# Performance work log

Hardware: AMD Instinct MI355X
Metric: run time of the kernel (lower is better)

Reference implementation:

```python
import jax, jax.numpy as jnp
import numpy as np
import math

B, C_IN, S, D, H, L, FF = 16, 32, 512, 256, 8, 4, 1024
HD = D // H
EPS = 1e-5


def setup_inputs() -> dict:
    key = jax.random.key(0)
    ks = jax.random.split(key, 32)
    r = lambda k, shp: jax.random.normal(k, shp, dtype=jnp.float32) * 0.02
    inp = {
        'x': jax.random.normal(ks[0], (B, C_IN, S), dtype=jnp.float32),
        'conv1_w': r(ks[1], (D, C_IN, 7)), 'conv1_b': jnp.zeros((D,)),
        'bn1_g': jnp.ones((D,)), 'bn1_b': jnp.zeros((D,)),
        'conv2_w': r(ks[2], (D, D, 5)), 'conv2_b': jnp.zeros((D,)),
        'bn2_g': jnp.ones((D,)), 'bn2_b': jnp.zeros((D,)),
        'ln1_g': jnp.ones((L, D)), 'ln1_b': jnp.zeros((L, D)),
        'wq': r(ks[3], (L, D, D)), 'wk': r(ks[4], (L, D, D)),
        'wv': r(ks[5], (L, D, D)), 'wo': r(ks[6], (L, D, D)),
        'bo': jnp.zeros((L, D)),
        'bias_table': r(ks[7], (L, 2 * S - 1, H)),
        'ln2_g': jnp.ones((L, D)), 'ln2_b': jnp.zeros((L, D)),
        'w1': r(ks[8], (L, D, FF)), 'b1': jnp.zeros((L, FF)),
        'w2': r(ks[9], (L, FF, D)), 'b2': jnp.zeros((L, D)),
        'fn_g': jnp.ones((D,)), 'fn_b': jnp.zeros((D,)),
    }
    return inp


def _conv1d(x, w, b, pad):
    # x: (B, C, T), w: (O, I, K) -> (B, O, T)
    y = jax.lax.conv_general_dilated(x, w, (1,), [(pad, pad)],
                                     dimension_numbers=('NCH', 'OIH', 'NCH'))
    return y + b[None, :, None]


def _bn_eval(x, g, b):
    # eval-mode batchnorm with running mean 0, var 1
    return x * (g / jnp.sqrt(1.0 + EPS))[None, :, None] + b[None, :, None]


def _ln(x, g, b):
    mu = jnp.mean(x, axis=-1, keepdims=True)
    var = jnp.var(x, axis=-1, keepdims=True)
    return (x - mu) / jnp.sqrt(var + EPS) * g + b


def _pos_encoding():
    pos = np.arange(S, dtype=np.float32)[:, None]
    div = np.exp(np.arange(0, D, 2, dtype=np.float32) * (-math.log(10000.0) / D))
    scale = D / S
    pe = np.zeros((S, D), dtype=np.float32)
    pe[:, 0::2] = np.sin(pos * div * scale)
    pe[:, 1::2] = np.cos(pos * div * scale)
    return jnp.asarray(pe)


_REL_IDX = jnp.asarray(np.arange(S)[:, None] - np.arange(S)[None, :] + S - 1)  # (S,S)
_PE = _pos_encoding()


def reference(x, conv1_w, conv1_b, bn1_g, bn1_b, conv2_w, conv2_b, bn2_g, bn2_b,
              ln1_g, ln1_b, wq, wk, wv, wo, bo, bias_table,
              ln2_g, ln2_b, w1, b1, w2, b2, fn_g, fn_b):
    # tokenizer
    h = jax.nn.gelu(_bn_eval(_conv1d(x, conv1_w, conv1_b, 3), bn1_g, bn1_b), approximate=False)
    h = jax.nn.gelu(_bn_eval(_conv1d(h, conv2_w, conv2_b, 2), bn2_g, bn2_b), approximate=False)
    t = jnp.transpose(h, (0, 2, 1))  # (B, S, D)
    # positional encoding
    t = t + _PE[None, :, :]
    scale = HD ** -0.5
    for i in range(L):
        xn = _ln(t, ln1_g[i], ln1_b[i])
        q = (xn @ wq[i]).reshape(B, S, H, HD)
        k = (xn @ wk[i]).reshape(B, S, H, HD)
        v = (xn @ wv[i]).reshape(B, S, H, HD)
        scores = jnp.einsum('bihd,bjhd->bhij', q, k) * scale
        rel = bias_table[i][_REL_IDX]              # (S, S, H)
        scores = scores + jnp.transpose(rel, (2, 0, 1))[None]
        probs = jax.nn.softmax(scores, axis=-1)
        ctx = jnp.einsum('bhij,bjhd->bihd', probs, v).reshape(B, S, D)
        t = t + ctx @ wo[i] + bo[i]
        xn2 = _ln(t, ln2_g[i], ln2_b[i])
        ff = jax.nn.gelu(xn2 @ w1[i] + b1[i], approximate=False) @ w2[i] + b2[i]
        t = t + ff
    return _ln(t, fn_g, fn_b)
```

## Files before the change

kernel.cpp:

```cpp
#include <hip/hip_runtime.h>
#include <hip/hip_bf16.h>
#include <stdint.h>

#define B_   16
#define CIN_ 32
#define S_   512
#define D_   256
#define H_   8
#define L_   4
#define FF_  1024
#define HD_  32
#define EPS_ 1e-5f

typedef __hip_bfloat16 bf16;
typedef __attribute__((ext_vector_type(8))) short short8;
typedef __attribute__((ext_vector_type(4))) float floatx4;

__device__ __forceinline__ float b2f(bf16 v) { return __bfloat162float(v); }
__device__ __forceinline__ bf16 f2b(float v) { return __float2bfloat16(v); }
__device__ __forceinline__ float gelu_f(float v) {
    return 0.5f * v * (1.0f + erff(v * 0.70710678118654752f));
}
__device__ __forceinline__ float pe_val(int s, int d) {
    int m2 = d & ~1;
    float div = expf((float)m2 * (-9.210340371976184f / 256.0f));
    float ang = (float)s * div * 0.5f;
    return (d & 1) ? cosf(ang) : sinf(ang);
}
__device__ __forceinline__ float us2f(unsigned short u) {
    return __uint_as_float(((unsigned)u) << 16);
}

__device__ __forceinline__ void wtrans_tile(const float* __restrict__ src, bf16* __restrict__ dst,
                                            int K, int N, int n0, int k0, int rowoff,
                                            const float* __restrict__ gvec,
                                            float (*tile)[33], int tid) {
    int tx = tid & 31, ty0 = tid >> 5;
#pragma unroll
    for (int r = 0; r < 4; ++r) {
        int ky = r * 8 + ty0;
        tile[ky][tx] = src[(long)(k0 + ky) * N + n0 + tx];
    }
    __syncthreads();
    float gs = gvec ? gvec[k0 + tx] : 1.0f;
#pragma unroll
    for (int r = 0; r < 4; ++r) {
        int ny = r * 8 + ty0;
        dst[(long)(rowoff + n0 + ny) * K + k0 + tx] = f2b(tile[tx][ny] * gs);
    }
}

__global__ void prep_kernel(const float* __restrict__ wq, const float* __restrict__ wk,
                            const float* __restrict__ wv, const float* __restrict__ wo,
                            const float* __restrict__ w1, const float* __restrict__ w2,
                            const float* __restrict__ ln1_g, const float* __restrict__ ln1_b,
                            const float* __restrict__ ln2_g, const float* __restrict__ ln2_b,
                            bf16* __restrict__ wqkvT, bf16* __restrict__ woT,
                            bf16* __restrict__ w1T, bf16* __restrict__ w2T,
                            const float* __restrict__ w1c, const float* __restrict__ cb1,
                            const float* __restrict__ g1, const float* __restrict__ bb1,
                            const float* __restrict__ w2c, const float* __restrict__ cb2,
                            const float* __restrict__ g2, const float* __restrict__ bb2,
                            bf16* __restrict__ c1w, bf16* __restrict__ c2w,
                            float* __restrict__ sh1, float* __restrict__ sh2,
                            float* __restrict__ zpage,
                            float* __restrict__ gWq, float* __restrict__ bWq,
                            float* __restrict__ gWf, float* __restrict__ bWf) {
    __shared__ float tile[32][33];
    int tid = threadIdx.x;
    int bid = blockIdx.x;
    if (bid < 3072) {
        int l = bid / 768, r = bid % 768;
        if (r < 256) {
            int which = r >> 6, rr = r & 63;
            int n0 = (rr & 7) * 32, k0 = (rr >> 3) * 32;
            const float* s = (which == 0 ? wq : which == 1 ? wk : which == 2 ? wv : wo) + (long)l * 65536;
            bf16* d = (which == 3) ? (woT + (long)l * 65536) : (wqkvT + (long)l * 768 * 256);
            const float* gv = (which == 3) ? nullptr : (ln1_g + l * 256);
            wtrans_tile(s, d, 256, 256, n0, k0, (which == 3) ? 0 : which * 256, gv, tile, tid);
        } else if (r < 512) {
            int rr = r - 256;
            int n0 = (rr & 31) * 32, k0 = (rr >> 5) * 32;
            wtrans_tile(w1 + (long)l * 262144, w1T + (long)l * 262144, 256, 1024, n0, k0, 0,
                        ln2_g + l * 256, tile, tid);
        } else {
            int rr = r - 512;
            int n0 = (rr & 7) * 32, k0 = (rr >> 3) * 32;
            wtrans_tile(w2 + (long)l * 262144, w2T + (long)l * 262144, 1024, 256, n0, k0, 0,
                        nullptr, tile, tid);
        }
        return;
    }
    if (bid >= 3105) {
        int j = bid - 3105;
        int l = j / 7, r = j % 7;
        int n = tid;
        if (r < 3) {
            const float* W = (r == 0 ? wq : r == 1 ? wk : wv) + (long)l * 65536;
            const float* g = ln1_g + l * 256;
            const float* bb = ln1_b + l * 256;
            float sg = 0.0f, sb = 0.0f;
            for (int k = 0; k < 256; ++k) {
                float w = W[k * 256 + n];
                sg += g[k] * w;
                sb += bb[k] * w;
            }
            gWq[l * 768 + r * 256 + n] = sg;
            bWq[l * 768 + r * 256 + n] = sb;
        } else {
            int c = r - 3;
            const float* W = w1 + (long)l * 262144;
            const float* g = ln2_g + l * 256;
            const float* bb = ln2_b + l * 256;
            float sg = 0.0f, sb = 0.0f;
            for (int k = 0; k < 256; ++k) {
                float w = W[k * 1024 + c * 256 + n];
                sg += g[k] * w;
                sb += bb[k] * w;
            }
            gWf[l * 1024 + c * 256 + n] = sg;
            bWf[l * 1024 + c * 256 + n] = sb;
        }
        return;
    }
    int cb = bid - 3072;
    int ty = tid >> 4, t16 = tid & 15;
    float rinv = rsqrtf(1.0f + EPS_);
    if (cb < 16) {
        int o = cb * 16 + ty;
        float scale = g1[o] * rinv;
        if (t16 == 0) sh1[o] = cb1[o] * scale + bb1[o];
        for (int j = t16; j < 256; j += 16) {
            int kk = j >> 5, i = j & 31;
            float v = (kk < 7) ? w1c[o * 224 + i * 7 + kk] * scale : 0.0f;
            c1w[o * 256 + kk * 32 + i] = f2b(v);
        }
    } else if (cb < 32) {
        int o = (cb - 16) * 16 + ty;
        float scale = g2[o] * rinv;
        if (t16 == 0) sh2[o] = cb2[o] * scale + bb2[o];
        for (int j = t16; j < D_ * 5; j += 16) {
            int i = j / 5, kk = j % 5;
            c2w[o * 1280 + kk * 256 + i] = f2b(w2c[o * 1280 + i * 5 + kk] * scale);
        }
    } else {
        if (tid < 64) zpage[tid] = 0.0f;
    }
}

__global__ void im2col1_kernel(const float* __restrict__ x, bf16* __restrict__ col) {
    int kk = blockIdx.x, b = blockIdx.y;
    for (int t = threadIdx.x; t < 512 * 32; t += 256) {
        int s = t & 511, i = t >> 9;
        int sp = s + kk - 3;
        float v = (kk < 7 && sp >= 0 && sp < 512) ? x[((b << 5) + i) * 512 + sp] : 0.0f;
        col[(long)((b << 9) + s) * 256 + kk * 32 + i] = f2b(v);
    }
}

__global__ void ln_kernel(const float* __restrict__ x, const float* __restrict__ g,
                          const float* __restrict__ bt, float* __restrict__ out_f) {
    int row = blockIdx.x;
    int tid = threadIdx.x;
    float v = x[(long)row * D_ + tid];
    float s1 = v, s2 = v * v;
    __shared__ float red[8];
#pragma unroll
    for (int off = 32; off; off >>= 1) {
        s1 += __shfl_xor(s1, off);
        s2 += __shfl_xor(s2, off);
    }
    int wave = tid >> 6;
    if ((tid & 63) == 0) { red[wave] = s1; red[4 + wave] = s2; }
    __syncthreads();
    if (tid == 0) {
        float a = red[0] + red[1] + red[2] + red[3];
        float q = red[4] + red[5] + red[6] + red[7];
        float mu = a * (1.0f / D_);
        float var = q * (1.0f / D_) - mu * mu;
        red[0] = mu;
        red[1] = rsqrtf(var + EPS_);
    }
    __syncthreads();
    out_f[(long)row * D_ + tid] = (v - red[0]) * red[1] * g[tid] + bt[tid];
}

template <int ROWS>
__device__ __forceinline__ void stage_sw(const char* gbase, long rs_bytes, int k_byte_off,
                                         char* lds_base, int tid) {
    constexpr int ROUNDS = ROWS / 32;
    char* lp = lds_base + (tid & 192) * 16;
#pragma unroll
    for (int r = 0; r < ROUNDS; ++r) {
        int s = r * 256 + tid;
        int row = s >> 3;
        int q = ((s & 7) ^ (row & 7)) * 16;
        const char* gp = gbase + (long)row * rs_bytes + k_byte_off + q;
        __builtin_amdgcn_global_load_lds((const __attribute__((address_space(1))) void*)gp,
                                         (__attribute__((address_space(3))) void*)(lp + r * 4096),
                                         16, 0, 0);
    }
}
__device__ __forceinline__ int sw_off(int m, int qc) {
    return m * 128 + ((qc ^ (m & 7)) * 16);
}

__device__ __forceinline__ void stage_c2(const char* h1b, int s0, int kt, const char* zp,
                                         char* lds_base, int tid) {
    int kk = kt >> 2;
    int c0 = (kt & 3) * 128;
    char* lp = lds_base + (tid & 192) * 16;
    int row = tid >> 3;
    int q = ((tid & 7) ^ (row & 7)) * 16;
    int sp = s0 + row + kk - 2;
    const char* gp = (sp >= 0 && sp < 512) ? h1b + (long)sp * 512 + c0 + q : zp + q;
    __builtin_amdgcn_global_load_lds((const __attribute__((address_space(1))) void*)gp,
                                     (__attribute__((address_space(3))) void*)lp, 16, 0, 0);
}

enum { FB = 1, FG = 2, FR = 4, FO16 = 8, FLN = 16, FW16 = 32 };

template <int BM, int NB, int FLAGS, bool VT>
__global__ __launch_bounds__(256) void gemm_sw(const bf16* __restrict__ A, const bf16* __restrict__ Wt,
                                               const float* __restrict__ bias, const float* __restrict__ res,
                                               const float* __restrict__ gW, const float* __restrict__ bW,
                                               float* __restrict__ outf, bf16* __restrict__ outb,
                                               bf16* __restrict__ out16, bf16* __restrict__ vt,
                                               int M, int N, int K) {
    constexpr int FM = BM / 32;
    __shared__ __align__(16) short As[2][BM * 64];
    __shared__ __align__(16) short Bs[2][64 * 64];
    __shared__ float mus[64], rstds[64];
    int tid = threadIdx.x;
    int wave = tid >> 6, lane = tid & 63;
    int frow = lane & 15, fquad = lane >> 4;
    int id = blockIdx.x;
    int m_low = id & 7;
    int s = id >> 3;
    int ni = s % NB;
    int mi = (s / NB) * 8 + m_low;
    int m0 = mi * BM, n0 = ni * 64;
    int wm = (wave & 1) * (BM / 2), wn = (wave >> 1) * 32;
    floatx4 acc[FM][2] = {};
    const char* Ab = (const char*)A + (long)m0 * K * 2;
    const char* Bb = (const char*)Wt + (long)n0 * K * 2;
    long rs = (long)K * 2;
    int KT = K >> 6;
    float s1 = 0.0f, s2 = 0.0f;
    int srow = tid >> 2, spart = tid & 3;
    stage_sw<BM>(Ab, rs, 0, (char*)As[0], tid);
    stage_sw<64>(Bb, rs, 0, (char*)Bs[0], tid);
    for (int kt = 0; kt < KT; ++kt) {
        int cur = kt & 1;
        __syncthreads();
        if (kt + 1 < KT) {
            stage_sw<BM>(Ab, rs, (kt + 1) * 128, (char*)As[1 - cur], tid);
            stage_sw<64>(Bb, rs, (kt + 1) * 128, (char*)Bs[1 - cur], tid);
        }
        const char* Ap = (const char*)As[cur];
        const char* Bp = (const char*)Bs[cur];
        if (FLAGS & FLN) {
#pragma unroll
            for (int c = 0; c < 2; ++c) {
                short8 v8 = *(const short8*)(Ap + sw_off(srow, spart * 2 + c));
#pragma unroll
                for (int e = 0; e < 8; ++e) {
                    float f = us2f((unsigned short)v8[e]);
                    s1 += f;
                    s2 += f * f;
                }
            }
        }
#pragma unroll
        for (int kh = 0; kh < 2; ++kh) {
            short8 af[FM], bw[2];
#pragma unroll
            for (int i = 0; i < FM; ++i)
                af[i] = *(const short8*)(Ap + sw_off(wm + i * 16 + frow, kh * 4 + fquad));
#pragma unroll
            for (int j = 0; j < 2; ++j)
                bw[j] = *(const short8*)(Bp + sw_off(wn + j * 16 + frow, kh * 4 + fquad));
#pragma unroll
            for (int i = 0; i < FM; ++i)
#pragma unroll
                for (int j = 0; j < 2; ++j)
                    acc[i][j] = __builtin_amdgcn_mfma_f32_16x16x32_bf16(af[i], bw[j], acc[i][j], 0, 0, 0);
        }
    }
    if (FLAGS & FLN) {
        s1 += __shfl_xor(s1, 1); s1 += __shfl_xor(s1, 2);
        s2 += __shfl_xor(s2, 1); s2 += __shfl_xor(s2, 2);
        if (spart == 0) {
            float mu = s1 * (1.0f / 256.0f);
            float var = s2 * (1.0f / 256.0f) - mu * mu;
            mus[srow] = mu;
            rstds[srow] = rsqrtf(var + EPS_);
        }
        __syncthreads();
    }
#pragma unroll
    for (int i = 0; i < FM; ++i) {
#pragma unroll
        for (int j = 0; j < 2; ++j) {
#pragma unroll
            for (int r = 0; r < 4; ++r) {
                int rl = wm + i * 16 + fquad * 4 + r;
                int row = m0 + rl;
                int col = n0 + wn + j * 16 + frow;
                float v = acc[i][j][r];
                if (FLAGS & FLN) {
                    float rsd = rstds[rl], mm = mus[rl];
                    v = v * rsd - rsd * mm * gW[col] + bW[col];
                }
                if (FLAGS & FB) v += bias[col];
                if (FLAGS & FG) v = gelu_f(v);
                if (FLAGS & FR) v += res[(long)row * N + col];
                if (VT) {
                    if (col < 512) {
                        outb[(long)row * 512 + col] = f2b(v);
                    } else {
                        int h = (col - 512) >> 5, d = col & 31;
                        int b = row >> 9, ss = row & 511;
                        vt[(long)((b * 8 + h) * 32 + d) * 512 + ss] = f2b(v);
                    }
                } else if (FLAGS & FO16) {
                    outb[(long)row * N + col] = f2b(v);
                } else {
                    outf[(long)row * N + col] = v;
                }
                if (FLAGS & FW16) out16[(long)row * N + col] = f2b(v);
            }
        }
    }
}

template <int NB>
__global__ __launch_bounds__(256) void gemm_c2(const bf16* __restrict__ h1, const bf16* __restrict__ c2w,
                                               const float* __restrict__ sh2, const float* __restrict__ zp,
                                               float* __restrict__ outf, bf16* __restrict__ out16) {
    __shared__ __align__(16) short As[2][32 * 64];
    __shared__ __align__(16) short Bs[2][64 * 64];
    int tid = threadIdx.x;
    int wave = tid >> 6, lane = tid & 63;
    int frow = lane & 15, fquad = lane >> 4;
    int id = blockIdx.x;
    int m_low = id & 7;
    int sdec = id >> 3;
    int ni = sdec % NB;
    int mi = (sdec / NB) * 8 + m_low;
    int m0 = mi * 32, n0 = ni * 64;
    int bb = m0 >> 9, s0 = m0 & 511;
    int wm = (wave & 1) * 16, wn = (wave >> 1) * 32;
    floatx4 acc[2] = {};
    const char* h1b = (const char*)h1 + (long)bb * 512 * 512;
    const char* Bb = (const char*)c2w + (long)n0 * 2560;
    stage_c2(h1b, s0, 0, (const char*)zp, (char*)As[0], tid);
    stage_sw<64>(Bb, 2560, 0, (char*)Bs[0], tid);
    for (int kt = 0; kt < 20; ++kt) {
        int cur = kt & 1;
        __syncthreads();
        if (kt + 1 < 20) {
            stage_c2(h1b, s0, kt + 1, (const char*)zp, (char*)As[1 - cur], tid);
            stage_sw<64>(Bb, 2560, (kt + 1) * 128, (char*)Bs[1 - cur], tid);
        }
        const char* Ap = (const char*)As[cur];
        const char* Bp = (const char*)Bs[cur];
#pragma unroll
        for (int kh = 0; kh < 2; ++kh) {
            short8 af, bw[2];
            af = *(const short8*)(Ap + sw_off(wm + frow, kh * 4 + fquad));
#pragma unroll
            for (int j = 0; j < 2; ++j)
                bw[j] = *(const short8*)(Bp + sw_off(wn + j * 16 + frow, kh * 4 + fquad));
#pragma unroll
            for (int j = 0; j < 2; ++j)
                acc[j] = __builtin_amdgcn_mfma_f32_16x16x32_bf16(af, bw[j], acc[j], 0, 0, 0);
        }
    }
#pragma unroll
    for (int j = 0; j < 2; ++j) {
#pragma unroll
        for (int r = 0; r < 4; ++r) {
            int row = m0 + wm + fquad * 4 + r;
            int col = n0 + wn + j * 16 + frow;
            float v = gelu_f(acc[j][r] + sh2[col]) + pe_val(row & 511, col);
            outf[(long)row * 256 + col] = v;
            out16[(long)row * 256 + col] = f2b(v);
        }
    }
}

#define PSTR2 72
__device__ __forceinline__ void stage_k(const char* gK, int j0, char* dst, int tid) {
    char* lp = dst + (tid & 192) * 16;
#pragma unroll
    for (int r = 0; r < 2; ++r) {
        int l = r * 256 + tid;
        int sr = l >> 3, cp = l & 7;
        int c = cp ^ (sr & 7);
        int j = sr * 2 + (c >> 2), cj = c & 3;
        const char* gp = gK + (long)(j0 + j) * 1024 + cj * 16;
        __builtin_amdgcn_global_load_lds((const __attribute__((address_space(1))) void*)gp,
                                         (__attribute__((address_space(3))) void*)(lp + r * 4096), 16, 0, 0);
    }
}
__device__ __forceinline__ void stage_v(const char* gV, int j0, char* dst, int tid) {
    char* lp = dst + (tid & 192) * 16;
#pragma unroll
    for (int r = 0; r < 2; ++r) {
        int l = r * 256 + tid;
        int row = l >> 4, cp = l & 15;
        int c = cp ^ (row & 7);
        const char* gp = gV + (long)row * 1024 + j0 * 2 + c * 16;
        __builtin_amdgcn_global_load_lds((const __attribute__((address_space(1))) void*)gp,
                                         (__attribute__((address_space(3))) void*)(lp + r * 4096), 16, 0, 0);
    }
}

__global__ __launch_bounds__(256) void fattn_kernel(const bf16* __restrict__ qk,
                                                    const bf16* __restrict__ Vt,
                                                    const float* __restrict__ bias_l,
                                                    bf16* __restrict__ ctx) {
    __shared__ __align__(16) char Ks[2][8192];
    __shared__ __align__(16) char Vs[2][8192];
    __shared__ __align__(16) short Ps[4 * 32 * PSTR2];
    __shared__ float bias_s[640];
    int tid = threadIdx.x;
    int wave = tid >> 6, lane = tid & 63;
    int frow = lane & 15, fquad = lane >> 4;
    int bh = blockIdx.y;
    int b = bh >> 3, h = bh & 7;
    int i0 = blockIdx.x * 128;
    int wm = wave * 32;
    const float scale = 0.17677669529663687f;

    for (int t = tid; t < 639; t += 256) bias_s[t] = bias_l[(i0 + t) * 8 + h];

    short8 qf[2];
#pragma unroll
    for (int i = 0; i < 2; ++i)
        qf[i] = *(const short8*)((const short*)qk +
                 (long)((b << 9) + i0 + wm + i * 16 + frow) * 512 + h * 32 + fquad * 8);

    const char* gK = (const char*)qk + (long)b * 512 * 1024 + 512 + h * 64;
    const char* gV = (const char*)Vt + (long)bh * 32 * 1024;

    floatx4 acc_o[2][2] = {};
    float run_m[2][4], run_l[2][4];
#pragma unroll
    for (int i = 0; i < 2; ++i)
#pragma unroll
        for (int r = 0; r < 4; ++r) { run_m[i][r] = -1e30f; run_l[i][r] = 0.0f; }

    short* Pw = Ps + wave * 32 * PSTR2;
    bf16* Pb = (bf16*)Pw;

    stage_k(gK, 0, Ks[0], tid);
    stage_v(gV, 0, Vs[0], tid);
    for (int tt = 0; tt < 4; ++tt) {
        int cur = tt & 1;
        int j0 = tt * 128;
        __syncthreads();
        if (tt + 1 < 4) {
            stage_k(gK, j0 + 128, Ks[1 - cur], tid);
            stage_v(gV, j0 + 128, Vs[1 - cur], tid);
        }
        const char* Kp = Ks[cur];
        const char* Vp = Vs[cur];

        floatx4 accs[2][8] = {};
#pragma unroll
        for (int jt = 0; jt < 8; ++jt) {
            int j = jt * 16 + frow;
            int sr = j >> 1;
            int c = ((j & 1) << 2) | fquad;
            short8 bk = *(const short8*)(Kp + sr * 128 + (c ^ (sr & 7)) * 16);
#pragma unroll
            for (int i = 0; i < 2; ++i)
                accs[i][jt] = __builtin_amdgcn_mfma_f32_16x16x32_bf16(qf[i], bk, accs[i][jt], 0, 0, 0);
        }
#pragma unroll
        for (int i = 0; i < 2; ++i) {
            int irel = wm + i * 16 + fquad * 4;
#pragma unroll
            for (int jt = 0; jt < 8; ++jt) {
                int jl = j0 + jt * 16 + frow;
#pragma unroll
                for (int r = 0; r < 4; ++r)
                    accs[i][jt][r] = accs[i][jt][r] * scale + bias_s[irel + r + 511 - jl];
            }
        }
#pragma unroll
        for (int i = 0; i < 2; ++i) {
#pragma unroll
            for (int r = 0; r < 4; ++r) {
                float m = -1e30f;
#pragma unroll
                for (int jt = 0; jt < 8; ++jt) m = fmaxf(m, accs[i][jt][r]);
                m = fmaxf(m, __shfl_xor(m, 1));
                m = fmaxf(m, __shfl_xor(m, 2));
                m = fmaxf(m, __shfl_xor(m, 4));
                m = fmaxf(m, __shfl_xor(m, 8));
                float nm = fmaxf(run_m[i][r], m);
                float al = __expf(run_m[i][r] - nm);
                run_m[i][r] = nm;
                float ts = 0.0f;
#pragma unroll
                for (int jt = 0; jt < 8; ++jt) {
                    float p = __expf(accs[i][jt][r] - nm);
                    accs[i][jt][r] = p;
                    ts += p;
                }
                ts += __shfl_xor(ts, 1);
                ts += __shfl_xor(ts, 2);
                ts += __shfl_xor(ts, 4);
                ts += __shfl_xor(ts, 8);
                run_l[i][r] = run_l[i][r] * al + ts;
                acc_o[i][0][r] *= al;
                acc_o[i][1][r] *= al;
            }
        }
#pragma unroll
        for (int ss = 0; ss < 2; ++ss) {
#pragma unroll
            for (int i = 0; i < 2; ++i)
#pragma unroll
                for (int j2 = 0; j2 < 4; ++j2)
#pragma unroll
                    for (int r = 0; r < 4; ++r)
                        Pb[(i * 16 + fquad * 4 + r) * PSTR2 + j2 * 16 + frow] =
                            f2b(accs[i][ss * 4 + j2][r]);
#pragma unroll
            for (int ksub = 0; ksub < 2; ++ksub) {
                short8 ap[2], bv[2];
#pragma unroll
                for (int i = 0; i < 2; ++i)
                    ap[i] = *(const short8*)(Pw + (i * 16 + frow) * PSTR2 + ksub * 32 + fquad * 8);
#pragma unroll
                for (int dt = 0; dt < 2; ++dt) {
                    int row = dt * 16 + frow;
                    int c = ss * 8 + ksub * 4 + fquad;
                    bv[dt] = *(const short8*)(Vp + row * 256 + (c ^ (row & 7)) * 16);
                }
#pragma unroll
                for (int i = 0; i < 2; ++i)
#pragma unroll
                    for (int dt = 0; dt < 2; ++dt)
                        acc_o[i][dt] = __builtin_amdgcn_mfma_f32_16x16x32_bf16(ap[i], bv[dt], acc_o[i][dt], 0, 0, 0);
            }
        }
    }

#pragma unroll
    for (int i = 0; i < 2; ++i) {
#pragma unroll
        for (int r = 0; r < 4; ++r) {
            float inv = 1.0f / run_l[i][r];
            int row = i0 + wm + i * 16 + fquad * 4 + r;
#pragma unroll
            for (int dt = 0; dt < 2; ++dt) {
                int d = dt * 16 + frow;
                ctx[(long)((b << 9) + row) * 256 + h * 32 + d] = f2b(acc_o[i][dt][r] * inv);
            }
        }
    }
}

extern "C" void kernel_launch(void* const* d_in, const int* in_sizes, int n_in,
                              void* d_out, int out_size, void* d_ws, size_t ws_size,
                              hipStream_t stream) {
    const float* x        = (const float*)d_in[0];
    const float* conv1_w  = (const float*)d_in[1];
    const float* conv1_b  = (const float*)d_in[2];
    const float* bn1_g    = (const float*)d_in[3];
    const float* bn1_b    = (const float*)d_in[4];
    const float* conv2_w  = (const float*)d_in[5];
    const float* conv2_b  = (const float*)d_in[6];
    const float* bn2_g    = (const float*)d_in[7];
    const float* bn2_b    = (const float*)d_in[8];
    const float* ln1_g    = (const float*)d_in[9];
    const float* ln1_b    = (const float*)d_in[10];
    const float* wq       = (const float*)d_in[11];
    const float* wk       = (const float*)d_in[12];
    const float* wv       = (const float*)d_in[13];
    const float* wo       = (const float*)d_in[14];
    const float* bo       = (const float*)d_in[15];
    const float* bias_tab = (const float*)d_in[16];
    const float* ln2_g    = (const float*)d_in[17];
    const float* ln2_b    = (const float*)d_in[18];
    const float* w1       = (const float*)d_in[19];
    const float* b1       = (const float*)d_in[20];
    const float* w2       = (const float*)d_in[21];
    const float* b2       = (const float*)d_in[22];
    const float* fn_g     = (const float*)d_in[23];
    const float* fn_b     = (const float*)d_in[24];
    (void)in_sizes; (void)n_in; (void)out_size; (void)ws_size;

    const int M = B_ * S_;
    char* wsb = (char*)d_ws;
    float* t    = (float*)wsb;
    bf16* qk    = (bf16*)(wsb + (8u << 20));
    bf16* h1    = (bf16*)(wsb + (8u << 20));
    char* reg2  = wsb + (16u << 20);
    bf16* Vt    = (bf16*)reg2;
    bf16* ff1   = (bf16*)reg2;
    bf16* col1  = (bf16*)reg2;
    bf16* t16   = (bf16*)(wsb + (36u << 20));
    bf16* ctx   = (bf16*)(wsb + (40u << 20));
    bf16* wqkvT = (bf16*)(wsb + (44u << 20));
    bf16* woT   = wqkvT + (long)L_ * 768 * 256;
    bf16* w1T   = woT + (long)L_ * 256 * 256;
    bf16* w2T   = w1T + (long)L_ * 1024 * 256;
    bf16* c1w   = w2T + (long)L_ * 256 * 1024;
    bf16* c2w   = c1w + 256 * 256;
    float* sh1  = (float*)(c2w + 256 * 1280);
    float* sh2  = sh1 + 256;
    float* zp   = sh2 + 256;
    float* gWq  = zp + 64;
    float* bWq  = gWq + L_ * 768;
    float* gWf  = bWq + L_ * 768;
    float* bWf  = gWf + L_ * 1024;

    prep_kernel<<<3133, 256, 0, stream>>>(wq, wk, wv, wo, w1, w2,
                                          ln1_g, ln1_b, ln2_g, ln2_b,
                                          wqkvT, woT, w1T, w2T,
                                          conv1_w, conv1_b, bn1_g, bn1_b,
                                          conv2_w, conv2_b, bn2_g, bn2_b,
                                          c1w, c2w, sh1, sh2, zp,
                                          gWq, bWq, gWf, bWf);

    im2col1_kernel<<<dim3(8, B_), 256, 0, stream>>>(x, col1);
    gemm_sw<32, 4, FB | FG | FO16, false><<<1024, 256, 0, stream>>>(
        col1, c1w, sh1, nullptr, nullptr, nullptr, nullptr, h1, nullptr, nullptr, M, 256, 256);
    gemm_c2<4><<<1024, 256, 0, stream>>>(h1, c2w, sh2, zp, t, t16);

    for (int l = 0; l < L_; ++l) {
        gemm_sw<64, 12, FLN, true><<<1536, 256, 0, stream>>>(
            t16, wqkvT + (long)l * 768 * 256, nullptr, nullptr,
            gWq + l * 768, bWq + l * 768, nullptr, qk, nullptr, Vt, M, 768, 256);
        fattn_kernel<<<dim3(4, B_ * H_), 256, 0, stream>>>(
            qk, Vt, bias_tab + (long)l * (2 * S_ - 1) * H_, ctx);
        gemm_sw<32, 4, FB | FR | FW16, false><<<1024, 256, 0, stream>>>(
            ctx, woT + (long)l * 65536, bo + l * D_, t, nullptr, nullptr,
            t, nullptr, t16, nullptr, M, 256, 256);
        gemm_sw<64, 16, FLN | FB | FG | FO16, false><<<2048, 256, 0, stream>>>(
            t16, w1T + (long)l * 262144, b1 + l * FF_, nullptr,
            gWf + l * 1024, bWf + l * 1024, nullptr, ff1, nullptr, nullptr, M, 1024, 256);
        gemm_sw<32, 4, FB | FR | FW16, false><<<1024, 256, 0, stream>>>(
            ff1, w2T + (long)l * 262144, b2 + l * D_, t, nullptr, nullptr,
            t, nullptr, t16, nullptr, M, 256, 1024);
    }
    ln_kernel<<<M, 256, 0, stream>>>(t, fn_g, fn_b, (float*)d_out);
}
```

Measured before the change: 499.9 us.

## Add single-stage K=256 GEMM kernel with whole-K LDS tile for small-K projections

Adds a gemm_k256 kernel that loads the entire 256-wide K dimension of a 32-row A tile and a 64-row B tile into LDS in one staged load with its own swizzle, then runs eight MFMA steps with no double-buffered loop or per-step barriers. LayerNorm statistics are computed once from the full staged row before the MFMAs, instead of being accumulated across K steps. QKV and FF1 move from 64-row to 32-row tiles, which doubles their grid sizes, while the conv1, Wo and FF1 paths use the new kernel and FF2 keeps the pipelined kernel specialised to BM=32. The whole-K tile uses 48KB of LDS, which may lower occupancy, and exposed load latency is no longer overlapped with compute.

```diff
diff --git a/kernel.cpp b/kernel.cpp
--- a/kernel.cpp
+++ b/kernel.cpp
@@ -205,6 +205,26 @@
     return m * 128 + ((qc ^ (m & 7)) * 16);
 }
 
+template <int ROWS>
+__device__ __forceinline__ void stage_rm(const char* gbase, long rs_bytes, char* lds_base, int tid) {
+    constexpr int ROUNDS = ROWS / 8;
+    char* lp = lds_base + (tid & 192) * 16;
+#pragma unroll
+    for (int r = 0; r < ROUNDS; ++r) {
+        int l = r * 256 + tid;
+        int row = l >> 5;
+        int cp = l & 31;
+        int c = (cp & ~7) | ((cp ^ row) & 7);
+        const char* gp = gbase + (long)row * rs_bytes + c * 16;
+        __builtin_amdgcn_global_load_lds((const __attribute__((address_space(1))) void*)gp,
+                                         (__attribute__((address_space(3))) void*)(lp + r * 4096),
+                                         16, 0, 0);
+    }
+}
+__device__ __forceinline__ int rm_off(int m, int qc) {
+    return m * 512 + (((qc & ~7) | ((qc ^ m) & 7)) * 16);
+}
+
 __device__ __forceinline__ void stage_c2(const char* h1b, int s0, int kt, const char* zp,
                                          char* lds_base, int tid) {
     int kk = kt >> 2;
@@ -220,17 +240,16 @@
 
 enum { FB = 1, FG = 2, FR = 4, FO16 = 8, FLN = 16, FW16 = 32 };
 
-template <int BM, int NB, int FLAGS, bool VT>
-__global__ __launch_bounds__(256) void gemm_sw(const bf16* __restrict__ A, const bf16* __restrict__ Wt,
-                                               const float* __restrict__ bias, const float* __restrict__ res,
-                                               const float* __restrict__ gW, const float* __restrict__ bW,
-                                               float* __restrict__ outf, bf16* __restrict__ outb,
-                                               bf16* __restrict__ out16, bf16* __restrict__ vt,
-                                               int M, int N, int K) {
-    constexpr int FM = BM / 32;
-    __shared__ __align__(16) short As[2][BM * 64];
-    __shared__ __align__(16) short Bs[2][64 * 64];
-    __shared__ float mus[64], rstds[64];
+template <int NB, int FLAGS, bool VT>
+__global__ __launch_bounds__(256) void gemm_k256(const bf16* __restrict__ A, const bf16* __restrict__ Wt,
+                                                 const float* __restrict__ bias, const float* __restrict__ res,
+                                                 const float* __restrict__ gW, const float* __restrict__ bW,
+                                                 float* __restrict__ outf, bf16* __restrict__ outb,
+                                                 bf16* __restrict__ out16, bf16* __restrict__ vt,
+                                                 int M, int N) {
+    __shared__ __align__(16) short As[32 * 256];
+    __shared__ __align__(16) short Bs[64 * 256];
+    __shared__ float mus[32], rstds[32];
     int tid = threadIdx.x;
     int wave = tid >> 6, lane = tid & 63;
     int frow = lane & 15, fquad = lane >> 4;
@@ -239,97 +258,132 @@
     int s = id >> 3;
     int ni = s % NB;
     int mi = (s / NB) * 8 + m_low;
-    int m0 = mi * BM, n0 = ni * 64;
-    int wm = (wave & 1) * (BM / 2), wn = (wave >> 1) * 32;
-    floatx4 acc[FM][2] = {};
+    int m0 = mi * 32, n0 = ni * 64;
+    int wm = (wave & 1) * 16, wn = (wave >> 1) * 32;
+    const char* Ab = (const char*)A + (long)m0 * 512;
+    const char* Bb = (const char*)Wt + (long)n0 * 512;
+    stage_rm<32>(Ab, 512, (char*)As, tid);
+    stage_rm<64>(Bb, 512, (char*)Bs, tid);
+    __syncthreads();
+    if (FLAGS & FLN) {
+        int srow = tid >> 3, spart = tid & 7;
+        float s1 = 0.0f, s2 = 0.0f;
+#pragma unroll
+        for (int c = 0; c < 4; ++c) {
+            short8 v8 = *(const short8*)((const char*)As + rm_off(srow, spart * 4 + c));
+#pragma unroll
+            for (int e = 0; e < 8; ++e) {
+                float f = us2f((unsigned short)v8[e]);
+                s1 += f;
+                s2 += f * f;
+            }
+        }
+        s1 += __shfl_xor(s1, 1); s1 += __shfl_xor(s1, 2); s1 += __shfl_xor(s1, 4);
+        s2 += __shfl_xor(s2, 1); s2 += __shfl_xor(s2, 2); s2 += __shfl_xor(s2, 4);
+        if (spart == 0) {
+            float mu = s1 * (1.0f / 256.0f);
+            float var = s2 * (1.0f / 256.0f) - mu * mu;
+            mus[srow] = mu;
+            rstds[srow] = rsqrtf(var + EPS_);
+        }
+    }
+    floatx4 acc[2] = {};
+#pragma unroll
+    for (int kh = 0; kh < 8; ++kh) {
+        short8 af = *(const short8*)((const char*)As + rm_off(wm + frow, kh * 4 + fquad));
+        short8 bw0 = *(const short8*)((const char*)Bs + rm_off(wn + frow, kh * 4 + fquad));
+        short8 bw1 = *(const short8*)((const char*)Bs + rm_off(wn + 16 + frow, kh * 4 + fquad));
+        acc[0] = __builtin_amdgcn_mfma_f32_16x16x32_bf16(af, bw0, acc[0], 0, 0, 0);
+        acc[1] = __builtin_amdgcn_mfma_f32_16x16x32_bf16(af, bw1, acc[1], 0, 0, 0);
+    }
+    if (FLAGS & FLN) __syncthreads();
+#pragma unroll
+    for (int j = 0; j < 2; ++j) {
+#pragma unroll
+        for (int r = 0; r < 4; ++r) {
+            int rl = wm + fquad * 4 + r;
+            int row = m0 + rl;
+            int col = n0 + wn + j * 16 + frow;
+            float v = acc[j][r];
+            if (FLAGS & FLN) {
+                float rsd = rstds[rl], mm = mus[rl];
+                v = v * rsd - rsd * mm * gW[col] + bW[col];
+            }
+            if (FLAGS & FB) v += bias[col];
+            if (FLAGS & FG) v = gelu_f(v);
+            if (FLAGS & FR) v += res[(long)row * N + col];
+            if (VT) {
+                if (col < 512) {
+                    outb[(long)row * 512 + col] = f2b(v);
+                } else {
+                    int h = (col - 512) >> 5, d = col & 31;
+                    int b = row >> 9, ss = row & 511;
+                    vt[(long)((b * 8 + h) * 32 + d) * 512 + ss] = f2b(v);
+                }
+            } else if (FLAGS & FO16) {
+                outb[(long)row * N + col] = f2b(v);
+            } else {
+                outf[(long)row * N + col] = v;
+            }
+            if (FLAGS & FW16) out16[(long)row * N + col] = f2b(v);
+        }
+    }
+}
+
+template <int NB, int FLAGS>
+__global__ __launch_bounds__(256) void gemm_sw(const bf16* __restrict__ A, const bf16* __restrict__ Wt,
+                                               const float* __restrict__ bias, const float* __restrict__ res,
+                                               float* __restrict__ outf, bf16* __restrict__ out16,
+                                               int M, int N, int K) {
+    __shared__ __align__(16) short As[2][32 * 64];
+    __shared__ __align__(16) short Bs[2][64 * 64];
+    int tid = threadIdx.x;
+    int wave = tid >> 6, lane = tid & 63;
+    int frow = lane & 15, fquad = lane >> 4;
+    int id = blockIdx.x;
+    int m_low = id & 7;
+    int s = id >> 3;
+    int ni = s % NB;
+    int mi = (s / NB) * 8 + m_low;
+    int m0 = mi * 32, n0 = ni * 64;
+    int wm = (wave & 1) * 16, wn = (wave >> 1) * 32;
+    floatx4 acc[2] = {};
     const char* Ab = (const char*)A + (long)m0 * K * 2;
     const char* Bb = (const char*)Wt + (long)n0 * K * 2;
     long rs = (long)K * 2;
     int KT = K >> 6;
-    float s1 = 0.0f, s2 = 0.0f;
-    int srow = tid >> 2, spart = tid & 3;
-    stage_sw<BM>(Ab, rs, 0, (char*)As[0], tid);
+    stage_sw<32>(Ab, rs, 0, (char*)As[0], tid);
     stage_sw<64>(Bb, rs, 0, (char*)Bs[0], tid);
     for (int kt = 0; kt < KT; ++kt) {
         int cur = kt & 1;
         __syncthreads();
         if (kt + 1 < KT) {
-            stage_sw<BM>(Ab, rs, (kt + 1) * 128, (char*)As[1 - cur], tid);
+            stage_sw<32>(Ab, rs, (kt + 1) * 128, (char*)As[1 - cur], tid);
             stage_sw<64>(Bb, rs, (kt + 1) * 128, (char*)Bs[1 - cur], tid);
         }
         const char* Ap = (const char*)As[cur];
         const char* Bp = (const char*)Bs[cur];
-        if (FLAGS & FLN) {
-#pragma unroll
-            for (int c = 0; c < 2; ++c) {
-                short8 v8 = *(const short8*)(Ap + sw_off(srow, spart * 2 + c));
-#pragma unroll
-                for (int e = 0; e < 8; ++e) {
-                    float f = us2f((unsigned short)v8[e]);
-                    s1 += f;
-                    s2 += f * f;
-                }
-            }
-        }
 #pragma unroll
         for (int kh = 0; kh < 2; ++kh) {
-            short8 af[FM], bw[2];
-#pragma unroll
-            for (int i = 0; i < FM; ++i)
-                af[i] = *(const short8*)(Ap + sw_off(wm + i * 16 + frow, kh * 4 + fquad));
-#pragma unroll
-            for (int j = 0; j < 2; ++j)
-                bw[j] = *(const short8*)(Bp + sw_off(wn + j * 16 + frow, kh * 4 + fquad));
-#pragma unroll
-            for (int i = 0; i < FM; ++i)
-#pragma unroll
-                for (int j = 0; j < 2; ++j)
-                    acc[i][j] = __builtin_amdgcn_mfma_f32_16x16x32_bf16(af[i], bw[j], acc[i][j], 0, 0, 0);
-        }
-    }
-    if (FLAGS & FLN) {
-        s1 += __shfl_xor(s1, 1); s1 += __shfl_xor(s1, 2);
-        s2 += __shfl_xor(s2, 1); s2 += __shfl_xor(s2, 2);
-        if (spart == 0) {
-            float mu = s1 * (1.0f / 256.0f);
-            float var = s2 * (1.0f / 256.0f) - mu * mu;
-            mus[srow] = mu;
-            rstds[srow] = rsqrtf(var + EPS_);
-        }
-        __syncthreads();
-    }
-#pragma unroll
-    for (int i = 0; i < FM; ++i) {
-#pragma unroll
-        for (int j = 0; j < 2; ++j) {
-#pragma unroll
-            for (int r = 0; r < 4; ++r) {
-                int rl = wm + i * 16 + fquad * 4 + r;
-                int row = m0 + rl;
-                int col = n0 + wn + j * 16 + frow;
-                float v = acc[i][j][r];
-                if (FLAGS & FLN) {
-                    float rsd = rstds[rl], mm = mus[rl];
-                    v = v * rsd - rsd * mm * gW[col] + bW[col];
-                }
-                if (FLAGS & FB) v += bias[col];
-                if (FLAGS & FG) v = gelu_f(v);
-                if (FLAGS & FR) v += res[(long)row * N + col];
-                if (VT) {
-                    if (col < 512) {
-                        outb[(long)row * 512 + col] = f2b(v);
-                    } else {
-                        int h = (col - 512) >> 5, d = col & 31;
-                        int b = row >> 9, ss = row & 511;
-                        vt[(long)((b * 8 + h) * 32 + d) * 512 + ss] = f2b(v);
-                    }
-                } else if (FLAGS & FO16) {
-                    outb[(long)row * N + col] = f2b(v);
-                } else {
-                    outf[(long)row * N + col] = v;
-                }
-                if (FLAGS & FW16) out16[(long)row * N + col] = f2b(v);
-            }
+            short8 af = *(const short8*)(Ap + sw_off(wm + frow, kh * 4 + fquad));
+            short8 bw0 = *(const short8*)(Bp + sw_off(wn + frow, kh * 4 + fquad));
+            short8 bw1 = *(const short8*)(Bp + sw_off(wn + 16 + frow, kh * 4 + fquad));
+            acc[0] = __builtin_amdgcn_mfma_f32_16x16x32_bf16(af, bw0, acc[0], 0, 0, 0);
+            acc[1] = __builtin_amdgcn_mfma_f32_16x16x32_bf16(af, bw1, acc[1], 0, 0, 0);
+        }
+    }
+#pragma unroll
+    for (int j = 0; j < 2; ++j) {
+#pragma unroll
+        for (int r = 0; r < 4; ++r) {
+            int row = m0 + wm + fquad * 4 + r;
+            int col = n0 + wn + j * 16 + frow;
+            float v = acc[j][r];
+            if (FLAGS & FB) v += bias[col];
+            if (FLAGS & FG) v = gelu_f(v);
+            if (FLAGS & FR) v += res[(long)row * N + col];
+            outf[(long)row * N + col] = v;
+            if (FLAGS & FW16) out16[(long)row * N + col] = f2b(v);
         }
     }
 }
@@ -367,14 +421,11 @@
         const char* Bp = (const char*)Bs[cur];
 #pragma unroll
         for (int kh = 0; kh < 2; ++kh) {
-            short8 af, bw[2];
-            af = *(const short8*)(Ap + sw_off(wm + frow, kh * 4 + fquad));
-#pragma unroll
-            for (int j = 0; j < 2; ++j)
-                bw[j] = *(const short8*)(Bp + sw_off(wn + j * 16 + frow, kh * 4 + fquad));
-#pragma unroll
-            for (int j = 0; j < 2; ++j)
-                acc[j] = __builtin_amdgcn_mfma_f32_16x16x32_bf16(af, bw[j], acc[j], 0, 0, 0);
+            short8 af = *(const short8*)(Ap + sw_off(wm + frow, kh * 4 + fquad));
+            short8 bw0 = *(const short8*)(Bp + sw_off(wn + frow, kh * 4 + fquad));
+            short8 bw1 = *(const short8*)(Bp + sw_off(wn + 16 + frow, kh * 4 + fquad));
+            acc[0] = __builtin_amdgcn_mfma_f32_16x16x32_bf16(af, bw0, acc[0], 0, 0, 0);
+            acc[1] = __builtin_amdgcn_mfma_f32_16x16x32_bf16(af, bw1, acc[1], 0, 0, 0);
         }
     }
 #pragma unroll
@@ -630,25 +681,24 @@
                                           gWq, bWq, gWf, bWf);
 
     im2col1_kernel<<<dim3(8, B_), 256, 0, stream>>>(x, col1);
-    gemm_sw<32, 4, FB | FG | FO16, false><<<1024, 256, 0, stream>>>(
-        col1, c1w, sh1, nullptr, nullptr, nullptr, nullptr, h1, nullptr, nullptr, M, 256, 256);
+    gemm_k256<4, FB | FG | FO16, false><<<1024, 256, 0, stream>>>(
+        col1, c1w, sh1, nullptr, nullptr, nullptr, nullptr, h1, nullptr, nullptr, M, 256);
     gemm_c2<4><<<1024, 256, 0, stream>>>(h1, c2w, sh2, zp, t, t16);
 
     for (int l = 0; l < L_; ++l) {
-        gemm_sw<64, 12, FLN, true><<<1536, 256, 0, stream>>>(
+        gemm_k256<12, FLN, true><<<3072, 256, 0, stream>>>(
             t16, wqkvT + (long)l * 768 * 256, nullptr, nullptr,
-            gWq + l * 768, bWq + l * 768, nullptr, qk, nullptr, Vt, M, 768, 256);
+            gWq + l * 768, bWq + l * 768, nullptr, qk, nullptr, Vt, M, 768);
         fattn_kernel<<<dim3(4, B_ * H_), 256, 0, stream>>>(
             qk, Vt, bias_tab + (long)l * (2 * S_ - 1) * H_, ctx);
-        gemm_sw<32, 4, FB | FR | FW16, false><<<1024, 256, 0, stream>>>(
-            ctx, woT + (long)l * 65536, bo + l * D_, t, nullptr, nullptr,
-            t, nullptr, t16, nullptr, M, 256, 256);
-        gemm_sw<64, 16, FLN | FB | FG | FO16, false><<<2048, 256, 0, stream>>>(
+        gemm_k256<4, FB | FR | FW16, false><<<1024, 256, 0, stream>>>(
+            ctx, woT + (long)l * 65536, bo + l * D_, t,
+            nullptr, nullptr, t, nullptr, t16, nullptr, M, 256);
+        gemm_k256<16, FLN | FB | FG | FO16, false><<<4096, 256, 0, stream>>>(
             t16, w1T + (long)l * 262144, b1 + l * FF_, nullptr,
-            gWf + l * 1024, bWf + l * 1024, nullptr, ff1, nullptr, nullptr, M, 1024, 256);
-        gemm_sw<32, 4, FB | FR | FW16, false><<<1024, 256, 0, stream>>>(
-            ff1, w2T + (long)l * 262144, b2 + l * D_, t, nullptr, nullptr,
-            t, nullptr, t16, nullptr, M, 256, 1024);
+            gWf + l * 1024, bWf + l * 1024, nullptr, ff1, nullptr, nullptr, M, 1024);
+        gemm_sw<4, FB | FR | FW16><<<1024, 256, 0, stream>>>(
+            ff1, w2T + (long)l * 262144, b2 + l * D_, t, t, t16, M, 256, 1024);
     }
     ln_kernel<<<M, 256, 0, stream>>>(t, fn_g, fn_b, (float*)d_out);
 }
```

Measured after the change: 533.2 us. 1.07x slower.
